# Kernel optimization log

Measured on AMD Instinct MI355X. Metric: run time of the kernel, lower is better.

Reference implementation:

```python
import jax, jax.numpy as jnp
import numpy as np

N = 100000       # nodes
E = 1600000      # edges
NFEAT = 128
NHID = 128
NCLASS = 64
NHEAD = 4
NLAYER = 3
LRELU_ALPHA = 0.2


def setup_inputs() -> dict:
    key = jax.random.key(0)
    ks = jax.random.split(key, 7)
    x = jax.random.normal(ks[0], (N, NFEAT), jnp.float32)
    edge_index = jax.random.randint(ks[1], (2, E), 0, N, jnp.int32)
    # xavier-uniform-ish init scales (gain for relu baked into scale roughly)
    Win = jax.random.normal(ks[2], (NFEAT, NHID), jnp.float32) * (2.0 / (NFEAT + NHID)) ** 0.5
    b_in = jnp.zeros((NHID,), jnp.float32)
    # per hidden layer, per head: a split into (src, dst) halves of the (1, 2*in) vector
    a_hid = jax.random.normal(ks[3], (NLAYER - 1, NHEAD, 2, NHID), jnp.float32) * 0.1
    W_hid = jax.random.normal(ks[4], (NLAYER - 1, NHEAD, NHID, NHID // NHEAD), jnp.float32) * (2.0 / (NHID + NHID // NHEAD)) ** 0.5
    a_out = jax.random.normal(ks[5], (2, NHID), jnp.float32) * 0.1
    W_out = jax.random.normal(ks[6], (NHID, NCLASS), jnp.float32) * (2.0 / (NHID + NCLASS)) ** 0.5
    return dict(x=x, edge_index=edge_index, Win=Win, b_in=b_in,
                a_hid=a_hid, W_hid=W_hid, a_out=a_out, W_out=W_out)


def _segment_softmax(logits, seg, n):
    # numerically stable softmax over groups defined by seg (axis 0)
    m = jax.ops.segment_max(logits, seg, num_segments=n)
    e = jnp.exp(logits - m[seg])
    s = jax.ops.segment_sum(e, seg, num_segments=n)
    return e / s[seg]


def _gat_conv(h, row, col, a, W):
    # h: [N, D]; a: [H, 2, D]; W: [H, D, Dh]
    n = h.shape[0]
    H = a.shape[0]
    s_src = h @ a[:, 0, :].T  # [N, H]
    s_dst = h @ a[:, 1, :].T  # [N, H]
    logits = jax.nn.leaky_relu(s_src[row] + s_dst[col], LRELU_ALPHA)  # [E, H]
    alpha = _segment_softmax(logits, row, n)  # softmax grouped by row (edge_index[0])
    h_col = h[col]  # [E, D] gathered once, reused per head
    outs = []
    for hd in range(H):  # small fixed head loop keeps peak memory at [E, D]
        agg = jax.ops.segment_sum(alpha[:, hd, None] * h_col, row, num_segments=n)  # [N, D]
        outs.append(agg @ W[hd])  # weight applied AFTER aggregation, as in source
    return jnp.concatenate(outs, axis=1)


def reference(x, edge_index, Win, b_in, a_hid, W_hid, a_out, W_out):
    row, col = edge_index[0], edge_index[1]
    h = jax.nn.elu(x @ Win + b_in)  # in_linear + ELU (dropout is identity in eval/p=0)
    for l in range(a_hid.shape[0]):
        h = jax.nn.elu(_gat_conv(h, row, col, a_hid[l], W_hid[l]))
    # final conv: single head to nclass, no activation
    return _gat_conv(h, row, col, a_out[None], W_out[None])
```

## Files before the change

kernel.cpp:

```cpp
#include <hip/hip_runtime.h>
#include <hip/hip_bf16.h>
#include <cstdint>
#include <cstddef>

#define LRELU_ALPHA 0.2f

typedef __attribute__((ext_vector_type(8))) short short8;
typedef __attribute__((ext_vector_type(4))) float f32x4;

__device__ __forceinline__ unsigned short f2bf(float f) {
    unsigned int u = __float_as_uint(f);
    unsigned int r = (u + 0x7fffu + ((u >> 16) & 1u)) >> 16;
    return (unsigned short)r;
}
__device__ __forceinline__ float bf2f(unsigned int lo16) {
    return __uint_as_float(lo16 << 16);
}
__device__ __forceinline__ unsigned int pk2(float a, float b) {
    return (unsigned int)f2bf(a) | ((unsigned int)f2bf(b) << 16);
}


__global__ void hist_k(const int* __restrict__ ei, int* __restrict__ counts,
                       int* __restrict__ rank, int E_) {
    int e = blockIdx.x * 256 + threadIdx.x;
    if (e < E_) {
        int r = ei[e];
        rank[e] = atomicAdd(&counts[r], 1);
    }
}

__global__ void scan_block_k(const int* __restrict__ counts, int* __restrict__ tmp,
                             int* __restrict__ bsum, int n) {
    __shared__ int s[256];
    int i = blockIdx.x * 256 + threadIdx.x;
    int v = (i < n) ? counts[i] : 0;
    s[threadIdx.x] = v;
    __syncthreads();
    for (int d = 1; d < 256; d <<= 1) {
        int t_ = (threadIdx.x >= d) ? s[threadIdx.x - d] : 0;
        __syncthreads();
        s[threadIdx.x] += t_;
        __syncthreads();
    }
    if (i < n) tmp[i] = s[threadIdx.x];
    if (threadIdx.x == 255) bsum[blockIdx.x] = s[255];
}

__global__ void scan_sums_k(int* bsum, int nb) {
    __shared__ int s[512];
    int v = ((int)threadIdx.x < nb) ? bsum[threadIdx.x] : 0;
    s[threadIdx.x] = v;
    __syncthreads();
    for (int d = 1; d < 512; d <<= 1) {
        int t_ = ((int)threadIdx.x >= d) ? s[threadIdx.x - d] : 0;
        __syncthreads();
        s[threadIdx.x] += t_;
        __syncthreads();
    }
    if ((int)threadIdx.x < nb) bsum[threadIdx.x] = s[threadIdx.x] - v;
}

__global__ void finalize_k(const int* __restrict__ tmp, const int* __restrict__ bsum,
                           int* __restrict__ off, int n) {
    int i = blockIdx.x * 256 + threadIdx.x;
    if (i < n) off[i + 1] = tmp[i] + bsum[blockIdx.x];
    if (i == 0) off[0] = 0;
}

__global__ void scatter_k(const int* __restrict__ ei, const int* __restrict__ rank,
                          const int* __restrict__ off, int* __restrict__ scol, int E_) {
    int e = blockIdx.x * 256 + threadIdx.x;
    if (e < E_) {
        int r = ei[e];
        int pos = off[r] + rank[e];
        scol[pos] = ei[E_ + e];
    }
}


template <int KJ, int HD>
__global__ void repack_wt(const float* __restrict__ src, unsigned short* __restrict__ wt) {
    int i = blockIdx.x * 256 + threadIdx.x;
    if (i < KJ * 128) {
        int n = i >> 7, k = i & 127;
        constexpr int JW = KJ / HD;
        int hd = n / JW, j = n % JW;
        wt[i] = f2bf(src[(hd * 128 + k) * JW + j]);
    }
}


template <int KJ, bool ELU_ACT, bool BIAS, bool BF16_OUT, bool ABF16>
__global__ __launch_bounds__(256) void gemm_mfma(const void* __restrict__ Xv,
                                                 const unsigned short* __restrict__ WT,
                                                 const float* __restrict__ bias,
                                                 void* __restrict__ Yv, int nRows) {
    constexpr int NT = KJ / 16;
    constexpr int WS = 136;
    __shared__ unsigned short sWT[KJ * WS];
    int t = threadIdx.x;
    for (int i = t; i < KJ * 16; i += 256) {
        int n = i >> 4, k8 = i & 15;
        uint4 v = *(const uint4*)&WT[n * 128 + k8 * 8];
        *(uint4*)&sWT[n * WS + k8 * 8] = v;
    }
    __syncthreads();

    int lane = t & 63;
    int wv = t >> 6;
    int m0 = blockIdx.x * 128 + wv * 32;
    int l16 = lane & 15;
    int q4 = lane >> 4;

    short8 afr[4][2];
    #pragma unroll
    for (int rt = 0; rt < 2; rt++) {
        int row = m0 + rt * 16 + l16;
        bool vr = row < nRows;
        if (ABF16) {
            const unsigned int* xp = (const unsigned int*)Xv + (size_t)row * 64 + q4 * 4;
            #pragma unroll
            for (int kk = 0; kk < 4; kk++) {
                uint4 u = make_uint4(0u, 0u, 0u, 0u);
                if (vr) u = *(const uint4*)(xp + kk * 16);
                afr[kk][rt] = *(short8*)&u;
            }
        } else {
            const float* xp = (const float*)Xv + (size_t)row * 128 + q4 * 8;
            #pragma unroll
            for (int kk = 0; kk < 4; kk++) {
                float4 a0 = make_float4(0.f, 0.f, 0.f, 0.f), a1 = a0;
                if (vr) {
                    a0 = *(const float4*)(xp + kk * 32);
                    a1 = *(const float4*)(xp + kk * 32 + 4);
                }
                unsigned int u[4];
                u[0] = pk2(a0.x, a0.y); u[1] = pk2(a0.z, a0.w);
                u[2] = pk2(a1.x, a1.y); u[3] = pk2(a1.z, a1.w);
                afr[kk][rt] = *(short8*)u;
            }
        }
    }

    f32x4 acc[2][NT] = {};
    #pragma unroll
    for (int kk = 0; kk < 4; kk++) {
        #pragma unroll
        for (int ct = 0; ct < NT; ct++) {
            int n = ct * 16 + l16;
            short8 bf = *(const short8*)&sWT[n * WS + kk * 32 + q4 * 8];
            #pragma unroll
            for (int rt = 0; rt < 2; rt++)
                acc[rt][ct] = __builtin_amdgcn_mfma_f32_16x16x32_bf16(afr[kk][rt], bf, acc[rt][ct], 0, 0, 0);
        }
    }

    #pragma unroll
    for (int rt = 0; rt < 2; rt++) {
        #pragma unroll
        for (int q = 0; q < 4; q++) {
            int row = m0 + rt * 16 + q4 * 4 + q;
            if (row >= nRows) continue;
            #pragma unroll
            for (int ct = 0; ct < NT; ct++) {
                int colc = ct * 16 + l16;
                float v = acc[rt][ct][q];
                if (BIAS) v += bias[colc];
                if (ELU_ACT) v = v > 0.f ? v : (__expf(v) - 1.f);
                if (BF16_OUT) ((unsigned short*)Yv)[(size_t)row * KJ + colc] = f2bf(v);
                else          ((float*)Yv)[(size_t)row * KJ + colc] = v;
            }
        }
    }
}


template <int H>
__global__ __launch_bounds__(256) void attn_scores_bf(const unsigned int* __restrict__ h2,
                                                      const float* __restrict__ a,
                                                      float* __restrict__ s_src,
                                                      float* __restrict__ s_dst, int n) {
    __shared__ float sa[H * 2 * 128];
    for (int i = threadIdx.x; i < H * 2 * 128; i += 256) sa[i] = a[i];
    __syncthreads();
    int lane = threadIdx.x & 63, wv = threadIdx.x >> 6;
    int node = blockIdx.x * 4 + wv;
    if (node >= n) return;
    unsigned int hv = h2[(size_t)node * 64 + lane];
    float v0 = bf2f(hv & 0xffffu), v1 = bf2f(hv >> 16);
    #pragma unroll
    for (int hd = 0; hd < H; hd++) {
        #pragma unroll
        for (int side = 0; side < 2; side++) {
            const float2 aa = *(const float2*)&sa[(hd * 2 + side) * 128 + 2 * lane];
            float p = v0 * aa.x + v1 * aa.y;
            #pragma unroll
            for (int s = 32; s > 0; s >>= 1) p += __shfl_xor(p, s);
            if (lane == 0) {
                float* dst = side ? s_dst : s_src;
                dst[node * H + hd] = p;
            }
        }
    }
}


template <int DHT, int H, bool ELU_ACT, int HN, bool BF16O>
__global__ __launch_bounds__(256) void edge_agg_v(const unsigned int* __restrict__ hW2,
                                                  const float* __restrict__ ssrc,
                                                  const float* __restrict__ sdst,
                                                  const int* __restrict__ off,
                                                  const int* __restrict__ scol,
                                                  void* __restrict__ outv,
                                                  const float* __restrict__ a_next,
                                                  float* __restrict__ ssrc_n,
                                                  float* __restrict__ sdst_n, int nRows) {
    constexpr int FPL = DHT / 16;
    constexpr int UPL = FPL / 2;
    constexpr int NC = (HN > 0) ? 2 * HN : 1;
    __shared__ float sAN[NC * 128];
    if (HN > 0) {
        for (int i = threadIdx.x; i < NC * 128; i += 256) sAN[i] = a_next[i];
        __syncthreads();
    }
    int lane = threadIdx.x & 63;
    int sub = lane & 15;
    int g = lane >> 4;
    int wv = threadIdx.x >> 6;
    int r = __builtin_amdgcn_readfirstlane(blockIdx.x * 4 + wv);
    if (r >= nRows) return;
    int begin = off[r], end = off[r + 1];

    int head = (H == 4) ? (sub >> 2) : 0;
    float ssl = ssrc[r * H + head];

    float acc[FPL] = {};
    float den = 0.f;

    for (int i = begin; i < end; i += 8) {
        int iA = i + g, iB = i + 4 + g;
        bool vA = iA < end, vB = iB < end;
        int cA = scol[vA ? iA : begin];
        int cB = scol[vB ? iB : begin];
        float sdA = sdst[cA * H + head];
        float sdB = sdst[cB * H + head];
        unsigned int hA[UPL], hB[UPL];
        int oA = cA * (DHT / 2) + sub * UPL;
        int oB = cB * (DHT / 2) + sub * UPL;
        if (UPL == 4) {
            *(uint4*)hA = *(const uint4*)&hW2[oA];
            *(uint4*)hB = *(const uint4*)&hW2[oB];
        } else {
            *(uint2*)hA = *(const uint2*)&hW2[oA];
            *(uint2*)hB = *(const uint2*)&hW2[oB];
        }
        float lgA = ssl + sdA; lgA = lgA > 0.f ? lgA : LRELU_ALPHA * lgA;
        float wA = vA ? __expf(lgA) : 0.f;
        float lgB = ssl + sdB; lgB = lgB > 0.f ? lgB : LRELU_ALPHA * lgB;
        float wB = vB ? __expf(lgB) : 0.f;
        den += wA + wB;
        #pragma unroll
        for (int q = 0; q < UPL; q++) {
            acc[2 * q]     = fmaf(wA, bf2f(hA[q] & 0xffffu), acc[2 * q]);
            acc[2 * q + 1] = fmaf(wA, bf2f(hA[q] >> 16),     acc[2 * q + 1]);
            acc[2 * q]     = fmaf(wB, bf2f(hB[q] & 0xffffu), acc[2 * q]);
            acc[2 * q + 1] = fmaf(wB, bf2f(hB[q] >> 16),     acc[2 * q + 1]);
        }
    }

    #pragma unroll
    for (int s = 16; s < 64; s <<= 1) {
        den += __shfl_xor(den, s);
        #pragma unroll
        for (int p = 0; p < FPL; p++) acc[p] += __shfl_xor(acc[p], s);
    }
    float inv = den > 0.f ? 1.f / den : 0.f;

    float v[FPL];
    #pragma unroll
    for (int p = 0; p < FPL; p++) {
        float tv = acc[p] * inv;
        if (ELU_ACT) tv = tv > 0.f ? tv : (__expf(tv) - 1.f);
        v[p] = tv;
    }

    if (DHT == 128) {
        if (BF16O)
            ((unsigned int*)outv)[(size_t)r * 64 + sub * 4 + g] = pk2(v[2 * g], v[2 * g + 1]);
        else
            *(float2*)&((float*)outv)[(size_t)r * 128 + sub * 8 + 2 * g] =
                make_float2(v[2 * g], v[2 * g + 1]);
    } else {
        ((float*)outv)[(size_t)r * DHT + sub * FPL + g] = v[g];
    }

    if (HN > 0) {
        constexpr int CPG = (HN == 4) ? 2 : 1;
        #pragma unroll
        for (int cc = 0; cc < CPG; cc++) {
            int c = (HN == 4) ? (g * 2 + cc) : (g & 1);
            const float* ap = &sAN[c * 128 + sub * FPL];
            float partial = 0.f;
            #pragma unroll
            for (int p = 0; p < FPL; p++) partial += v[p] * ap[p];
            #pragma unroll
            for (int s = 1; s < 16; s <<= 1) partial += __shfl_xor(partial, s);
            if (sub == 0 && (HN == 4 || g < 2)) {
                int hd = c >> 1;
                float* dst = (c & 1) ? sdst_n : ssrc_n;
                dst[r * HN + hd] = partial;
            }
        }
    }
}


extern "C" void kernel_launch(void* const* d_in, const int* in_sizes, int n_in,
                              void* d_out, int out_size, void* d_ws, size_t ws_size,
                              hipStream_t stream) {
    const float* x    = (const float*)d_in[0];
    const int*   ei   = (const int*)d_in[1];
    const float* Win  = (const float*)d_in[2];
    const float* bin  = (const float*)d_in[3];
    const float* ahid = (const float*)d_in[4];
    const float* Whid = (const float*)d_in[5];
    const float* aout = (const float*)d_in[6];
    const float* Wout = (const float*)d_in[7];
    float* out = (float*)d_out;

    const int N_ = in_sizes[0] / 128;
    const int E_ = in_sizes[1] / 2;

    char* p = (char*)d_ws;
    auto alloc = [&](size_t bytes) {
        char* q = p;
        p += (bytes + 511) & ~(size_t)511;
        return q;
    };
    int* counts = (int*)alloc((size_t)N_ * 4);
    int* tmp    = (int*)alloc((size_t)N_ * 4);
    int* rank   = (int*)alloc((size_t)E_ * 4);
    int* off    = (int*)alloc((size_t)(N_ + 1) * 4);
    int* bsum   = (int*)alloc(4096);
    int* scol   = (int*)alloc((size_t)(E_ + 8) * 4);
    float* ssrcA = (float*)alloc((size_t)N_ * 4 * 4);
    float* sdstA = (float*)alloc((size_t)N_ * 4 * 4);
    float* ssrcB = (float*)alloc((size_t)N_ * 4 * 4);
    float* sdstB = (float*)alloc((size_t)N_ * 4 * 4);
    unsigned int* hb  = (unsigned int*)alloc((size_t)N_ * 64 * 4);
    unsigned int* hWb = (unsigned int*)alloc((size_t)N_ * 64 * 4);
    unsigned short* WTb = (unsigned short*)alloc(128 * 128 * 2);

    int NB = (N_ + 255) / 256;
    int EB = (E_ + 255) / 256;
    int RT = (N_ + 127) / 128;
    int NW = (N_ + 3) / 4;

    hipMemsetAsync(counts, 0, (size_t)N_ * 4, stream);
    hist_k<<<EB, 256, 0, stream>>>(ei, counts, rank, E_);
    scan_block_k<<<NB, 256, 0, stream>>>(counts, tmp, bsum, N_);
    scan_sums_k<<<1, 512, 0, stream>>>(bsum, NB);
    finalize_k<<<NB, 256, 0, stream>>>(tmp, bsum, off, N_);
    scatter_k<<<EB, 256, 0, stream>>>(ei, rank, off, scol, E_);

    repack_wt<128, 1><<<64, 256, 0, stream>>>(Win, WTb);
    gemm_mfma<128, true, true, true, false><<<RT, 256, 0, stream>>>(x, WTb, bin, hb, N_);

    attn_scores_bf<4><<<NW, 256, 0, stream>>>(hb, ahid, ssrcA, sdstA, N_);

    repack_wt<128, 4><<<64, 256, 0, stream>>>(Whid, WTb);
    gemm_mfma<128, false, false, true, true><<<RT, 256, 0, stream>>>(hb, WTb, nullptr, hWb, N_);
    edge_agg_v<128, 4, true, 4, true><<<NW, 256, 0, stream>>>(
        hWb, ssrcA, sdstA, off, scol, hb, ahid + 4 * 2 * 128, ssrcB, sdstB, N_);

    repack_wt<128, 4><<<64, 256, 0, stream>>>(Whid + (size_t)4 * 128 * 32, WTb);
    gemm_mfma<128, false, false, true, true><<<RT, 256, 0, stream>>>(hb, WTb, nullptr, hWb, N_);
    edge_agg_v<128, 4, true, 1, true><<<NW, 256, 0, stream>>>(
        hWb, ssrcB, sdstB, off, scol, hb, aout, ssrcA, sdstA, N_);

    repack_wt<64, 1><<<32, 256, 0, stream>>>(Wout, WTb);
    gemm_mfma<64, false, false, true, true><<<RT, 256, 0, stream>>>(hb, WTb, nullptr, hWb, N_);
    edge_agg_v<64, 1, false, 0, false><<<NW, 256, 0, stream>>>(
        hWb, ssrcA, sdstA, off, scol, out, nullptr, nullptr, nullptr, N_);
}
```

Before: 522.6 us.

## Process two rows per wavefront in edge aggregation and batch weight prep

The edge aggregation kernel now handles two destination rows per wavefront, one per 32-lane half. Each half walks its own edge list in steps of four and skips the per-row bounds branching by padding scol with zeros. Source and destination attention scores are interleaved into a single [N,8] array so each lookup touches one cache line. The four weight repacks and the counts memset are merged into one prep kernel, and the histogram and scatter kernels each handle two edges per thread with int2 loads. The aim is less launch overhead, fewer idle lanes on low-degree rows, and more coalesced score access. The cost is divergence between the two halves when their rows have very different degrees.

```diff
diff --git a/kernel.cpp b/kernel.cpp
--- a/kernel.cpp
+++ b/kernel.cpp
@@ -21,12 +21,46 @@
 }
 
 
+__device__ __forceinline__ void repack_dev(const float* __restrict__ src,
+                                           unsigned short* __restrict__ wt,
+                                           int b, int KJ, int JW) {
+    int i = b * 256 + threadIdx.x;
+    if (i < KJ * 128) {
+        int n = i >> 7, k = i & 127;
+        int hd = n / JW, j = n % JW;
+        wt[i] = f2bf(src[(hd * 128 + k) * JW + j]);
+    }
+}
+
+__global__ void prep_k(const float* __restrict__ Win, const float* __restrict__ Whid,
+                       const float* __restrict__ Wout,
+                       unsigned short* __restrict__ WT0, unsigned short* __restrict__ WT1,
+                       unsigned short* __restrict__ WT2, unsigned short* __restrict__ WT3,
+                       int* __restrict__ counts, int* __restrict__ scol,
+                       int n, int E_, int nb) {
+    int b = blockIdx.x;
+    if (b < 64)       repack_dev(Win, WT0, b, 128, 128);
+    else if (b < 128) repack_dev(Whid, WT1, b - 64, 128, 32);
+    else if (b < 192) repack_dev(Whid + 4 * 128 * 32, WT2, b - 128, 128, 32);
+    else if (b < 224) repack_dev(Wout, WT3, b - 192, 64, 64);
+    else if (b < 224 + nb) {
+        int i = (b - 224) * 256 + threadIdx.x;
+        if (i < n) counts[i] = 0;
+    } else {
+        scol[E_ + threadIdx.x] = 0;
+    }
+}
+
+
 __global__ void hist_k(const int* __restrict__ ei, int* __restrict__ counts,
-                       int* __restrict__ rank, int E_) {
-    int e = blockIdx.x * 256 + threadIdx.x;
-    if (e < E_) {
-        int r = ei[e];
-        rank[e] = atomicAdd(&counts[r], 1);
+                       int* __restrict__ rank, int E2) {
+    int e2 = blockIdx.x * 256 + threadIdx.x;
+    if (e2 < E2) {
+        int2 rr = *(const int2*)&ei[e2 * 2];
+        int2 rk;
+        rk.x = atomicAdd(&counts[rr.x], 1);
+        rk.y = atomicAdd(&counts[rr.y], 1);
+        *(int2*)&rank[e2 * 2] = rk;
     }
 }
 
@@ -69,24 +103,14 @@
 }
 
 __global__ void scatter_k(const int* __restrict__ ei, const int* __restrict__ rank,
-                          const int* __restrict__ off, int* __restrict__ scol, int E_) {
-    int e = blockIdx.x * 256 + threadIdx.x;
-    if (e < E_) {
-        int r = ei[e];
-        int pos = off[r] + rank[e];
-        scol[pos] = ei[E_ + e];
-    }
-}
-
-
-template <int KJ, int HD>
-__global__ void repack_wt(const float* __restrict__ src, unsigned short* __restrict__ wt) {
-    int i = blockIdx.x * 256 + threadIdx.x;
-    if (i < KJ * 128) {
-        int n = i >> 7, k = i & 127;
-        constexpr int JW = KJ / HD;
-        int hd = n / JW, j = n % JW;
-        wt[i] = f2bf(src[(hd * 128 + k) * JW + j]);
+                          const int* __restrict__ off, int* __restrict__ scol, int E2) {
+    int e2 = blockIdx.x * 256 + threadIdx.x;
+    if (e2 < E2) {
+        int2 rr = *(const int2*)&ei[e2 * 2];
+        int2 rk = *(const int2*)&rank[e2 * 2];
+        int2 cc = *(const int2*)&ei[E2 * 2 + e2 * 2];
+        scol[off[rr.x] + rk.x] = cc.x;
+        scol[off[rr.y] + rk.y] = cc.y;
     }
 }
 
@@ -176,13 +200,11 @@
 }
 
 
-template <int H>
-__global__ __launch_bounds__(256) void attn_scores_bf(const unsigned int* __restrict__ h2,
-                                                      const float* __restrict__ a,
-                                                      float* __restrict__ s_src,
-                                                      float* __restrict__ s_dst, int n) {
-    __shared__ float sa[H * 2 * 128];
-    for (int i = threadIdx.x; i < H * 2 * 128; i += 256) sa[i] = a[i];
+__global__ __launch_bounds__(256) void attn0_bf(const unsigned int* __restrict__ h2,
+                                                const float* __restrict__ a,
+                                                float* __restrict__ sAB, int n) {
+    __shared__ float sa[8 * 128];
+    for (int i = threadIdx.x; i < 8 * 128; i += 256) sa[i] = a[i];
     __syncthreads();
     int lane = threadIdx.x & 63, wv = threadIdx.x >> 6;
     int node = blockIdx.x * 4 + wv;
@@ -190,32 +212,27 @@
     unsigned int hv = h2[(size_t)node * 64 + lane];
     float v0 = bf2f(hv & 0xffffu), v1 = bf2f(hv >> 16);
     #pragma unroll
-    for (int hd = 0; hd < H; hd++) {
+    for (int hd = 0; hd < 4; hd++) {
         #pragma unroll
         for (int side = 0; side < 2; side++) {
             const float2 aa = *(const float2*)&sa[(hd * 2 + side) * 128 + 2 * lane];
             float p = v0 * aa.x + v1 * aa.y;
             #pragma unroll
             for (int s = 32; s > 0; s >>= 1) p += __shfl_xor(p, s);
-            if (lane == 0) {
-                float* dst = side ? s_dst : s_src;
-                dst[node * H + hd] = p;
-            }
+            if (lane == 0) sAB[node * 8 + hd * 2 + side] = p;
         }
     }
 }
 
 
 template <int DHT, int H, bool ELU_ACT, int HN, bool BF16O>
-__global__ __launch_bounds__(256) void edge_agg_v(const unsigned int* __restrict__ hW2,
-                                                  const float* __restrict__ ssrc,
-                                                  const float* __restrict__ sdst,
+__global__ __launch_bounds__(256) void edge_agg2r(const unsigned int* __restrict__ hW2,
+                                                  const float* __restrict__ sAB,
                                                   const int* __restrict__ off,
                                                   const int* __restrict__ scol,
                                                   void* __restrict__ outv,
                                                   const float* __restrict__ a_next,
-                                                  float* __restrict__ ssrc_n,
-                                                  float* __restrict__ sdst_n, int nRows) {
+                                                  float* __restrict__ sABn, int nRows) {
     constexpr int FPL = DHT / 16;
     constexpr int UPL = FPL / 2;
     constexpr int NC = (HN > 0) ? 2 * HN : 1;
@@ -226,39 +243,44 @@
     }
     int lane = threadIdx.x & 63;
     int sub = lane & 15;
-    int g = lane >> 4;
+    int g = (lane >> 4) & 1;
+    int half = lane >> 5;
     int wv = threadIdx.x >> 6;
-    int r = __builtin_amdgcn_readfirstlane(blockIdx.x * 4 + wv);
-    if (r >= nRows) return;
-    int begin = off[r], end = off[r + 1];
+    int row = blockIdx.x * 8 + wv * 2 + half;
+    bool vrow = row < nRows;
+    int rowc = vrow ? row : 0;
+    int begin = off[rowc];
+    int end = vrow ? off[rowc + 1] : begin;
 
     int head = (H == 4) ? (sub >> 2) : 0;
-    float ssl = ssrc[r * H + head];
+    float ssl = sAB[rowc * 2 * H + head * 2];
+
+    int iters = (end - begin + 3) >> 2;
+    int o = __shfl_xor(iters, 32);
+    int itmax = iters > o ? iters : o;
 
     float acc[FPL] = {};
     float den = 0.f;
-
-    for (int i = begin; i < end; i += 8) {
-        int iA = i + g, iB = i + 4 + g;
-        bool vA = iA < end, vB = iB < end;
-        int cA = scol[vA ? iA : begin];
-        int cB = scol[vB ? iB : begin];
-        float sdA = sdst[cA * H + head];
-        float sdB = sdst[cB * H + head];
+    int idx0 = begin + g * 2;
+
+    for (int k = 0; k < itmax; k++) {
+        int iA = idx0 + k * 4, iB = iA + 1;
+        int cA = scol[iA];
+        int cB = scol[iB];
+        float sdA = sAB[cA * 2 * H + head * 2 + 1];
+        float sdB = sAB[cB * 2 * H + head * 2 + 1];
         unsigned int hA[UPL], hB[UPL];
-        int oA = cA * (DHT / 2) + sub * UPL;
-        int oB = cB * (DHT / 2) + sub * UPL;
         if (UPL == 4) {
-            *(uint4*)hA = *(const uint4*)&hW2[oA];
-            *(uint4*)hB = *(const uint4*)&hW2[oB];
+            *(uint4*)hA = *(const uint4*)&hW2[(size_t)cA * 64 + sub * 4];
+            *(uint4*)hB = *(const uint4*)&hW2[(size_t)cB * 64 + sub * 4];
         } else {
-            *(uint2*)hA = *(const uint2*)&hW2[oA];
-            *(uint2*)hB = *(const uint2*)&hW2[oB];
-        }
-        float lgA = ssl + sdA; lgA = lgA > 0.f ? lgA : LRELU_ALPHA * lgA;
-        float wA = vA ? __expf(lgA) : 0.f;
-        float lgB = ssl + sdB; lgB = lgB > 0.f ? lgB : LRELU_ALPHA * lgB;
-        float wB = vB ? __expf(lgB) : 0.f;
+            *(uint2*)hA = *(const uint2*)&hW2[(size_t)cA * 32 + sub * 2];
+            *(uint2*)hB = *(const uint2*)&hW2[(size_t)cB * 32 + sub * 2];
+        }
+        float lgA = ssl + sdA; lgA = fmaxf(lgA, LRELU_ALPHA * lgA);
+        float wA = (iA < end) ? __expf(lgA) : 0.f;
+        float lgB = ssl + sdB; lgB = fmaxf(lgB, LRELU_ALPHA * lgB);
+        float wB = (iB < end) ? __expf(lgB) : 0.f;
         den += wA + wB;
         #pragma unroll
         for (int q = 0; q < UPL; q++) {
@@ -269,12 +291,9 @@
         }
     }
 
-    #pragma unroll
-    for (int s = 16; s < 64; s <<= 1) {
-        den += __shfl_xor(den, s);
-        #pragma unroll
-        for (int p = 0; p < FPL; p++) acc[p] += __shfl_xor(acc[p], s);
-    }
+    den += __shfl_xor(den, 16);
+    #pragma unroll
+    for (int p = 0; p < FPL; p++) acc[p] += __shfl_xor(acc[p], 16);
     float inv = den > 0.f ? 1.f / den : 0.f;
 
     float v[FPL];
@@ -286,31 +305,50 @@
     }
 
     if (DHT == 128) {
-        if (BF16O)
-            ((unsigned int*)outv)[(size_t)r * 64 + sub * 4 + g] = pk2(v[2 * g], v[2 * g + 1]);
-        else
-            *(float2*)&((float*)outv)[(size_t)r * 128 + sub * 8 + 2 * g] =
-                make_float2(v[2 * g], v[2 * g + 1]);
+        if (vrow && g == 0) {
+            unsigned int pk[4];
+            #pragma unroll
+            for (int q = 0; q < 4; q++) pk[q] = pk2(v[2 * q], v[2 * q + 1]);
+            if (BF16O)
+                *(uint4*)&((unsigned int*)outv)[(size_t)row * 64 + sub * 4] = *(uint4*)pk;
+            else {
+                float4 f0 = make_float4(v[0], v[1], v[2], v[3]);
+                float4 f1 = make_float4(v[4], v[5], v[6], v[7]);
+                *(float4*)&((float*)outv)[(size_t)row * 128 + sub * 8] = f0;
+                *(float4*)&((float*)outv)[(size_t)row * 128 + sub * 8 + 4] = f1;
+            }
+        }
     } else {
-        ((float*)outv)[(size_t)r * DHT + sub * FPL + g] = v[g];
+        if (vrow && g == 0)
+            *(float4*)&((float*)outv)[(size_t)row * 64 + sub * 4] =
+                make_float4(v[0], v[1], v[2], v[3]);
     }
 
     if (HN > 0) {
-        constexpr int CPG = (HN == 4) ? 2 : 1;
-        #pragma unroll
-        for (int cc = 0; cc < CPG; cc++) {
-            int c = (HN == 4) ? (g * 2 + cc) : (g & 1);
-            const float* ap = &sAN[c * 128 + sub * FPL];
-            float partial = 0.f;
-            #pragma unroll
-            for (int p = 0; p < FPL; p++) partial += v[p] * ap[p];
-            #pragma unroll
-            for (int s = 1; s < 16; s <<= 1) partial += __shfl_xor(partial, s);
-            if (sub == 0 && (HN == 4 || g < 2)) {
-                int hd = c >> 1;
-                float* dst = (c & 1) ? sdst_n : ssrc_n;
-                dst[r * HN + hd] = partial;
+        if (HN == 4) {
+            float part[4];
+            #pragma unroll
+            for (int cc = 0; cc < 4; cc++) {
+                int ch = g * 4 + cc;
+                const float* ap = &sAN[ch * 128 + sub * FPL];
+                float pa = 0.f;
+                #pragma unroll
+                for (int p = 0; p < FPL; p++) pa += v[p] * ap[p];
+                #pragma unroll
+                for (int s = 1; s < 16; s <<= 1) pa += __shfl_xor(pa, s);
+                part[cc] = pa;
             }
+            if (vrow && sub == 0)
+                *(float4*)&sABn[(size_t)row * 8 + g * 4] =
+                    make_float4(part[0], part[1], part[2], part[3]);
+        } else {
+            const float* ap = &sAN[g * 128 + sub * FPL];
+            float pa = 0.f;
+            #pragma unroll
+            for (int p = 0; p < FPL; p++) pa += v[p] * ap[p];
+            #pragma unroll
+            for (int s = 1; s < 16; s <<= 1) pa += __shfl_xor(pa, s);
+            if (vrow && sub == 0) sABn[(size_t)row * 2 + g] = pa;
         }
     }
 }
@@ -331,6 +369,7 @@
 
     const int N_ = in_sizes[0] / 128;
     const int E_ = in_sizes[1] / 2;
+    const int E2 = E_ / 2;
 
     char* p = (char*)d_ws;
     auto alloc = [&](size_t bytes) {
@@ -343,44 +382,44 @@
     int* rank   = (int*)alloc((size_t)E_ * 4);
     int* off    = (int*)alloc((size_t)(N_ + 1) * 4);
     int* bsum   = (int*)alloc(4096);
-    int* scol   = (int*)alloc((size_t)(E_ + 8) * 4);
-    float* ssrcA = (float*)alloc((size_t)N_ * 4 * 4);
-    float* sdstA = (float*)alloc((size_t)N_ * 4 * 4);
-    float* ssrcB = (float*)alloc((size_t)N_ * 4 * 4);
-    float* sdstB = (float*)alloc((size_t)N_ * 4 * 4);
+    int* scol   = (int*)alloc((size_t)(E_ + 256) * 4);
+    float* sABa = (float*)alloc((size_t)N_ * 8 * 4);
+    float* sABb = (float*)alloc((size_t)N_ * 8 * 4);
     unsigned int* hb  = (unsigned int*)alloc((size_t)N_ * 64 * 4);
     unsigned int* hWb = (unsigned int*)alloc((size_t)N_ * 64 * 4);
-    unsigned short* WTb = (unsigned short*)alloc(128 * 128 * 2);
+    unsigned short* WT0 = (unsigned short*)alloc(128 * 128 * 2);
+    unsigned short* WT1 = (unsigned short*)alloc(128 * 128 * 2);
+    unsigned short* WT2 = (unsigned short*)alloc(128 * 128 * 2);
+    unsigned short* WT3 = (unsigned short*)alloc(64 * 128 * 2);
 
     int NB = (N_ + 255) / 256;
-    int EB = (E_ + 255) / 256;
+    int EB2 = (E2 + 255) / 256;
     int RT = (N_ + 127) / 128;
-    int NW = (N_ + 3) / 4;
-
-    hipMemsetAsync(counts, 0, (size_t)N_ * 4, stream);
-    hist_k<<<EB, 256, 0, stream>>>(ei, counts, rank, E_);
+    int NW4 = (N_ + 3) / 4;
+    int NW8 = (N_ + 7) / 8;
+
+    prep_k<<<224 + NB + 1, 256, 0, stream>>>(Win, Whid, Wout, WT0, WT1, WT2, WT3,
+                                             counts, scol, N_, E_, NB);
+
+    hist_k<<<EB2, 256, 0, stream>>>(ei, counts, rank, E2);
     scan_block_k<<<NB, 256, 0, stream>>>(counts, tmp, bsum, N_);
     scan_sums_k<<<1, 512, 0, stream>>>(bsum, NB);
     finalize_k<<<NB, 256, 0, stream>>>(tmp, bsum, off, N_);
-    scatter_k<<<EB, 256, 0, stream>>>(ei, rank, off, scol, E_);
-
-    repack_wt<128, 1><<<64, 256, 0, stream>>>(Win, WTb);
-    gemm_mfma<128, true, true, true, false><<<RT, 256, 0, stream>>>(x, WTb, bin, hb, N_);
-
-    attn_scores_bf<4><<<NW, 256, 0, stream>>>(hb, ahid, ssrcA, sdstA, N_);
-
-    repack_wt<128, 4><<<64, 256, 0, stream>>>(Whid, WTb);
-    gemm_mfma<128, false, false, true, true><<<RT, 256, 0, stream>>>(hb, WTb, nullptr, hWb, N_);
-    edge_agg_v<128, 4, true, 4, true><<<NW, 256, 0, stream>>>(
-        hWb, ssrcA, sdstA, off, scol, hb, ahid + 4 * 2 * 128, ssrcB, sdstB, N_);
-
-    repack_wt<128, 4><<<64, 256, 0, stream>>>(Whid + (size_t)4 * 128 * 32, WTb);
-    gemm_mfma<128, false, false, true, true><<<RT, 256, 0, stream>>>(hb, WTb, nullptr, hWb, N_);
-    edge_agg_v<128, 4, true, 1, true><<<NW, 256, 0, stream>>>(
-        hWb, ssrcB, sdstB, off, scol, hb, aout, ssrcA, sdstA, N_);
-
-    repack_wt<64, 1><<<32, 256, 0, stream>>>(Wout, WTb);
-    gemm_mfma<64, false, false, true, true><<<RT, 256, 0, stream>>>(hb, WTb, nullptr, hWb, N_);
-    edge_agg_v<64, 1, false, 0, false><<<NW, 256, 0, stream>>>(
-        hWb, ssrcA, sdstA, off, scol, out, nullptr, nullptr, nullptr, N_);
-}
+    scatter_k<<<EB2, 256, 0, stream>>>(ei, rank, off, scol, E2);
+
+    gemm_mfma<128, true, true, true, false><<<RT, 256, 0, stream>>>(x, WT0, bin, hb, N_);
+
+    attn0_bf<<<NW4, 256, 0, stream>>>(hb, ahid, sABa, N_);
+
+    gemm_mfma<128, false, false, true, true><<<RT, 256, 0, stream>>>(hb, WT1, nullptr, hWb, N_);
+    edge_agg2r<128, 4, true, 4, true><<<NW8, 256, 0, stream>>>(
+        hWb, sABa, off, scol, hb, ahid + 4 * 2 * 128, sABb, N_);
+
+    gemm_mfma<128, false, false, true, true><<<RT, 256, 0, stream>>>(hb, WT2, nullptr, hWb, N_);
+    edge_agg2r<128, 4, true, 1, true><<<NW8, 256, 0, stream>>>(
+        hWb, sABb, off, scol, hb, aout, sABa, N_);
+
+    gemm_mfma<64, false, false, true, true><<<RT, 256, 0, stream>>>(hb, WT3, nullptr, hWb, N_);
+    edge_agg2r<64, 1, false, 0, false><<<NW8, 256, 0, stream>>>(
+        hWb, sABa, off, scol, out, nullptr, nullptr, N_);
+}
```

Measured after the change: 543.4 us. 1.04x slower.
